# Performance work log

Hardware: AMD Instinct MI355X
Metric: run time of the kernel (lower is better)

## Reference

```python
import jax, jax.numpy as jnp
import numpy as np

N_CUST = 500000
N_FUND = 50000
N_EDGE = 4000000
D_CUST = 101
D_FUND = 1
HID = 64


def setup_inputs() -> dict:
    key = jax.random.key(0)
    ks = jax.random.split(key, 16)
    s = lambda fan_in: 1.0 / np.sqrt(fan_in)
    return {
        "x_customer": jax.random.normal(ks[0], (N_CUST, D_CUST), jnp.float32),
        "x_fund": jax.random.normal(ks[1], (N_FUND, D_FUND), jnp.float32),
        "src_fund": jax.random.randint(ks[2], (N_EDGE,), 0, N_FUND, jnp.int64),
        "dst_customer": jax.random.randint(ks[3], (N_EDGE,), 0, N_CUST, jnp.int64),
        # per-node-type input projections
        "W_cust": jax.random.uniform(ks[4], (D_CUST, HID), jnp.float32, -s(D_CUST), s(D_CUST)),
        "b_cust": jax.random.uniform(ks[5], (HID,), jnp.float32, -s(D_CUST), s(D_CUST)),
        "W_fund": jax.random.uniform(ks[6], (D_FUND, HID), jnp.float32, -s(D_FUND), s(D_FUND)),
        "b_fund": jax.random.uniform(ks[7], (HID,), jnp.float32, -s(D_FUND), s(D_FUND)),
        # SAGEConv fund->customer: lin_l (neighbor aggr, bias) + lin_r (self, no bias)
        "W_l": jax.random.uniform(ks[8], (HID, HID), jnp.float32, -s(HID), s(HID)),
        "b_l": jax.random.uniform(ks[9], (HID,), jnp.float32, -s(HID), s(HID)),
        "W_r": jax.random.uniform(ks[10], (HID, HID), jnp.float32, -s(HID), s(HID)),
        # output head
        "W_out": jax.random.uniform(ks[11], (HID, 2), jnp.float32, -s(HID), s(HID)),
        "b_out": jax.random.uniform(ks[12], (2,), jnp.float32, -s(HID), s(HID)),
    }


def reference(x_customer, x_fund, src_fund, dst_customer,
              W_cust, b_cust, W_fund, b_fund, W_l, b_l, W_r, W_out, b_out):
    # per-node-type linear + relu
    h_c = jax.nn.relu(x_customer @ W_cust + b_cust)  # [N_CUST, HID]
    h_f = jax.nn.relu(x_fund @ W_fund + b_fund)      # [N_FUND, HID]

    # SAGEConv (fund -> customer): gather src fund features per edge,
    # mean-aggregate by destination customer (scatter-sum / count)
    msgs = h_f[src_fund]  # [N_EDGE, HID]
    summed = jax.ops.segment_sum(msgs, dst_customer, num_segments=N_CUST)
    cnt = jax.ops.segment_sum(jnp.ones((msgs.shape[0],), msgs.dtype),
                              dst_customer, num_segments=N_CUST)
    mean = summed / jnp.maximum(cnt, 1.0)[:, None]

    out_c = mean @ W_l + b_l + h_c @ W_r  # SAGE: lin_l(aggr) + lin_r(self)
    return out_c @ W_out + b_out          # [N_CUST, 2]
```

## Files before the change

### kernel.cpp

```cpp
#include <hip/hip_runtime.h>
#include <stdint.h>

#define N_CUST 500000
#define N_FUND 50000
#define N_EDGE 4000000
#define D_CUST 101
#define HID 64

#define NB   512
#define EPB  ((N_EDGE + NB - 1) / NB)
#define CB   512
#define NBKT ((N_CUST + CB - 1) / CB)
#define CAP  5120
#define GPAD 32
#define LROW 104

typedef float float4u __attribute__((ext_vector_type(4), aligned(4)));
typedef float float4a __attribute__((ext_vector_type(4), aligned(16)));
using frag_ab = __attribute__((ext_vector_type(8))) short;
using frag_cd = __attribute__((ext_vector_type(4))) float;

struct __align__(16) Accum { float g0, g1, cnt, pad; };

__device__ __forceinline__ short f2bf(float f) {
    unsigned u = __float_as_uint(f);
    u += 0x7fffu + ((u >> 16) & 1u);
    return (short)(u >> 16);
}

__global__ __launch_bounds__(256) void k_gf(
    const float* __restrict__ x_fund,
    const float* __restrict__ W_fund,
    const float* __restrict__ b_fund,
    const float* __restrict__ W_l,
    const float* __restrict__ W_r,
    const float* __restrict__ W_out,
    const float* __restrict__ Wc,
    const float* __restrict__ b_l,
    const float* __restrict__ b_out,
    float2* __restrict__ gf,
    frag_ab* __restrict__ wcb,
    float* __restrict__ Bt,
    float* __restrict__ c2,
    unsigned* __restrict__ gcur,
    float4* __restrict__ Az)
{
    __shared__ float sAf[128];
    __shared__ float sWf[64];
    __shared__ float sBf[64];
    int t = threadIdx.x;

    if (Az != nullptr) {
        float4 z4 = make_float4(0.f, 0.f, 0.f, 0.f);
        for (int i = blockIdx.x * 256 + t; i < N_CUST; i += gridDim.x * 256)
            Az[i] = z4;
    }

    if (t < 128) {
        int h = t >> 1, j = t & 1;
        float s = 0.f;
        for (int k = 0; k < 64; ++k)
            s = fmaf(W_l[h * 64 + k], W_out[k * 2 + j], s);
        sAf[t] = s;
    } else if (t < 192) {
        sWf[t - 128] = W_fund[t - 128];
    } else {
        sBf[t - 192] = b_fund[t - 192];
    }
    __syncthreads();

    int f = blockIdx.x * 256 + t;
    if (f < N_FUND) {
        float xf = x_fund[f];
        float g0 = 0.f, g1 = 0.f;
        #pragma unroll
        for (int h = 0; h < 64; ++h) {
            float hf = fmaxf(fmaf(xf, sWf[h], sBf[h]), 0.f);
            g0 = fmaf(hf, sAf[2 * h + 0], g0);
            g1 = fmaf(hf, sAf[2 * h + 1], g1);
        }
        gf[f] = make_float2(g0, g1);
    }

    if (blockIdx.x == 0) {
        for (int k = t; k < NBKT * GPAD; k += 256) gcur[k] = 0u;
        if (t < 128) {
            int h = t >> 1, j = t & 1;
            float s = 0.f;
            for (int k = 0; k < 64; ++k)
                s = fmaf(W_r[h * 64 + k], W_out[k * 2 + j], s);
            Bt[t] = s;
        } else if (t < 130) {
            int j = t - 128;
            float s = b_out[j];
            for (int k = 0; k < 64; ++k)
                s = fmaf(b_l[k], W_out[k * 2 + j], s);
            c2[j] = s;
        }
        for (int sidx = t; sidx < 1024; sidx += 256) {
            int fidx = sidx >> 6, l = sidx & 63;
            int c = l & 15, q = l >> 4;
            int nt = fidx >> 2, kc = fidx & 3;
            frag_ab fr;
            #pragma unroll
            for (int j = 0; j < 8; ++j) {
                int kk = kc * 32 + q * 8 + j;
                int h  = nt * 16 + c;
                fr[j] = (kk < D_CUST) ? f2bf(Wc[kk * HID + h]) : (short)0;
            }
            wcb[sidx] = fr;
        }
    }
}

__global__ __launch_bounds__(512) void k_reorder(
    const int* __restrict__ src, const int* __restrict__ dst,
    unsigned* __restrict__ gcur, unsigned* __restrict__ recs)
{
    __shared__ unsigned hist[NBKT];
    __shared__ unsigned localOff[NBKT];
    __shared__ unsigned cur[NBKT];
    __shared__ unsigned baseG[NBKT];
    __shared__ unsigned ldsRec[EPB];
    __shared__ unsigned short ldsBkt[EPB];

    int t = threadIdx.x, b = blockIdx.x;
    int e0 = b * EPB, e1 = min(e0 + EPB, N_EDGE);
    int cntE = e1 - e0;

    for (int k = t; k < NBKT; k += 512) hist[k] = 0;
    __syncthreads();
    for (int e = e0 + t; e < e1; e += 512)
        atomicAdd(&hist[((unsigned)dst[e]) >> 9], 1u);
    __syncthreads();

    if (t < 64) {
        unsigned v[16], pre[16], run = 0;
        #pragma unroll
        for (int j = 0; j < 16; ++j) {
            int idx = t * 16 + j;
            v[j] = (idx < NBKT) ? hist[idx] : 0u;
            pre[j] = run; run += v[j];
        }
        unsigned sc = run;
        #pragma unroll
        for (int d = 1; d < 64; d <<= 1) {
            unsigned n = __shfl_up(sc, d, 64);
            if (t >= d) sc += n;
        }
        unsigned lane_excl = sc - run;
        #pragma unroll
        for (int j = 0; j < 16; ++j) {
            int idx = t * 16 + j;
            if (idx < NBKT) {
                localOff[idx] = lane_excl + pre[j];
                cur[idx]      = lane_excl + pre[j];
            }
        }
    }
    __syncthreads();

    for (int k = t; k < NBKT; k += 512) {
        unsigned h = hist[k];
        baseG[k] = h ? ((unsigned)k * CAP + atomicAdd(&gcur[k * GPAD], h)) : 0u;
    }

    for (int e = e0 + t; e < e1; e += 512) {
        unsigned d = (unsigned)dst[e];
        unsigned s = (unsigned)src[e];
        unsigned k = d >> 9;
        unsigned p = atomicAdd(&cur[k], 1u);
        ldsRec[p] = s | ((d & 511u) << 16);
        ldsBkt[p] = (unsigned short)k;
    }
    __syncthreads();

    for (int i = t; i < cntE; i += 512) {
        unsigned k = ldsBkt[i];
        unsigned g = baseG[k] + (i - localOff[k]);
        if (g < (k + 1u) * CAP) recs[g] = ldsRec[i];
    }
}

__global__ __launch_bounds__(256) void k_bucket(
    const unsigned* __restrict__ recs, const unsigned* __restrict__ gcur,
    const float2* __restrict__ gf,
    const float* __restrict__ x, const float* __restrict__ bc,
    const frag_ab* __restrict__ wcb, const float* __restrict__ Bt,
    const float* __restrict__ c2,
    float2* __restrict__ out)
{
    __shared__ float s0[CB], s1[CB], scn[CB];
    __shared__ float pbuf[2 * CB];
    __shared__ float xbuf[3][16 * LROW];

    int t = threadIdx.x, k = blockIdx.x;
    int w = t >> 6, lane = t & 63;
    int c = lane & 15, q = lane >> 4;

    for (int cc = t; cc < CB; cc += 256) { s0[cc] = 0.f; s1[cc] = 0.f; scn[cc] = 0.f; }
    __syncthreads();

    int cust0 = k * CB;
    int ncust = min(CB, N_CUST - cust0);
    int n_tiles = ncust >> 4;

    if (w == 3) {
        unsigned n = min(gcur[(unsigned)k * GPAD], (unsigned)CAP);
        const unsigned* rp = recs + (size_t)k * CAP;
        unsigned i = (unsigned)lane * 4u;
        for (; i + 4u <= n; i += 256u) {
            uint4 rr = *(const uint4*)(rp + i);
            float2 ga = gf[rr.x & 0xFFFFu];
            float2 gb = gf[rr.y & 0xFFFFu];
            float2 gc = gf[rr.z & 0xFFFFu];
            float2 gd = gf[rr.w & 0xFFFFu];
            unsigned da = rr.x >> 16, db = rr.y >> 16;
            unsigned dc = rr.z >> 16, dd = rr.w >> 16;
            atomicAdd(&s0[da], ga.x); atomicAdd(&s1[da], ga.y); atomicAdd(&scn[da], 1.f);
            atomicAdd(&s0[db], gb.x); atomicAdd(&s1[db], gb.y); atomicAdd(&scn[db], 1.f);
            atomicAdd(&s0[dc], gc.x); atomicAdd(&s1[dc], gc.y); atomicAdd(&scn[dc], 1.f);
            atomicAdd(&s0[dd], gd.x); atomicAdd(&s1[dd], gd.y); atomicAdd(&scn[dd], 1.f);
        }
        unsigned base = n & ~3u;
        if ((unsigned)lane < (n & 3u)) {
            unsigned r = rp[base + lane];
            float2 g = gf[r & 0xFFFFu];
            unsigned dl = r >> 16;
            atomicAdd(&s0[dl], g.x); atomicAdd(&s1[dl], g.y); atomicAdd(&scn[dl], 1.f);
        }
    } else {
        float* buf = xbuf[w];
        frag_ab bfrag[16];
        #pragma unroll
        for (int f = 0; f < 16; ++f) bfrag[f] = wcb[f * 64 + lane];
        float btv[8];
        #pragma unroll
        for (int nt = 0; nt < 4; ++nt) {
            btv[2 * nt]     = Bt[(nt * 16 + c) * 2];
            btv[2 * nt + 1] = Bt[(nt * 16 + c) * 2 + 1];
        }
        float bcv[4];
        #pragma unroll
        for (int nt = 0; nt < 4; ++nt) bcv[nt] = bc[nt * 16 + c];
        float c20 = c2[0], c21 = c2[1];

        int r = lane >> 2, s4 = lane & 3;

        for (int tl = w; tl < n_tiles; tl += 3) {
            const float* tb = x + (size_t)(cust0 + tl * 16) * D_CUST;
            #pragma unroll
            for (int rnd = 0; rnd < 7; ++rnd) {
                int ch = s4 + rnd * 4;
                if (ch < 25) {
                    float4u v = *(const float4u*)(tb + r * D_CUST + ch * 4);
                    *(float4a*)(buf + r * LROW + ch * 4) = v;
                } else if (ch == 25) {
                    buf[r * LROW + 100] = tb[r * D_CUST + 100];
                }
            }

            frag_ab af[4];
            #pragma unroll
            for (int kc = 0; kc < 3; ++kc) {
                float4a lo = *(const float4a*)(buf + c * LROW + kc * 32 + q * 8);
                float4a hi = *(const float4a*)(buf + c * LROW + kc * 32 + q * 8 + 4);
                frag_ab f;
                f[0]=f2bf(lo[0]); f[1]=f2bf(lo[1]); f[2]=f2bf(lo[2]); f[3]=f2bf(lo[3]);
                f[4]=f2bf(hi[0]); f[5]=f2bf(hi[1]); f[6]=f2bf(hi[2]); f[7]=f2bf(hi[3]);
                af[kc] = f;
            }
            {
                frag_ab f = {0,0,0,0,0,0,0,0};
                if (q == 0) {
                    float4a lo = *(const float4a*)(buf + c * LROW + 96);
                    f[0]=f2bf(lo[0]); f[1]=f2bf(lo[1]); f[2]=f2bf(lo[2]); f[3]=f2bf(lo[3]);
                    f[4]=f2bf(buf[c * LROW + 100]);
                }
                af[3] = f;
            }

            frag_cd acc[4];
            #pragma unroll
            for (int nt = 0; nt < 4; ++nt)
                acc[nt] = (frag_cd){bcv[nt], bcv[nt], bcv[nt], bcv[nt]};
            #pragma unroll
            for (int kc = 0; kc < 4; ++kc)
                #pragma unroll
                for (int nt = 0; nt < 4; ++nt)
                    acc[nt] = __builtin_amdgcn_mfma_f32_16x16x32_bf16(
                        af[kc], bfrag[nt * 4 + kc], acc[nt], 0, 0, 0);

            #pragma unroll
            for (int i = 0; i < 4; ++i) {
                float p0 = 0.f, p1 = 0.f;
                #pragma unroll
                for (int nt = 0; nt < 4; ++nt) {
                    float zv = fmaxf(acc[nt][i], 0.f);
                    p0 = fmaf(zv, btv[2 * nt],     p0);
                    p1 = fmaf(zv, btv[2 * nt + 1], p1);
                }
                #pragma unroll
                for (int m = 1; m < 16; m <<= 1) {
                    p0 += __shfl_xor(p0, m, 16);
                    p1 += __shfl_xor(p1, m, 16);
                }
                if (c == 0) {
                    int lrow = tl * 16 + q * 4 + i;
                    pbuf[2 * lrow]     = p0 + c20;
                    pbuf[2 * lrow + 1] = p1 + c21;
                }
            }
        }
    }
    __syncthreads();

    for (int cc = t; cc < ncust; cc += 256) {
        float inv = 1.0f / fmaxf(scn[cc], 1.0f);
        out[cust0 + cc] = make_float2(fmaf(s0[cc], inv, pbuf[2 * cc]),
                                      fmaf(s1[cc], inv, pbuf[2 * cc + 1]));
    }
}

__global__ __launch_bounds__(256) void k_scatter_direct(
    const int* __restrict__ src, const int* __restrict__ dst,
    const float2* __restrict__ gf, Accum* __restrict__ A)
{
    int stride = gridDim.x * 256;
    for (int e = blockIdx.x * 256 + threadIdx.x; e < N_EDGE; e += stride) {
        int s = src[e], d = dst[e];
        float2 g = gf[s];
        unsafeAtomicAdd(&A[d].g0, g.x);
        unsafeAtomicAdd(&A[d].g1, g.y);
        unsafeAtomicAdd(&A[d].cnt, 1.0f);
    }
}

__global__ __launch_bounds__(256) void k_mean(
    const Accum* __restrict__ A, float2* __restrict__ mean2)
{
    int i = blockIdx.x * 256 + threadIdx.x;
    if (i < N_CUST) {
        Accum a = A[i];
        float inv = 1.0f / fmaxf(a.cnt, 1.0f);
        mean2[i] = make_float2(a.g0 * inv, a.g1 * inv);
    }
}

__global__ __launch_bounds__(256) void k_gemm(
    const float* __restrict__ x, const float* __restrict__ bc,
    const frag_ab* __restrict__ wcb, const float* __restrict__ Bt,
    const float* __restrict__ c2, const float2* __restrict__ mean2,
    float2* __restrict__ out)
{
    __shared__ float sBt[128];
    __shared__ float zb[4][16 * 68];

    int t = threadIdx.x;
    int w = t >> 6, lane = t & 63;
    int c = lane & 15, q = lane >> 4;
    float* z = zb[w];

    if (t < 128) sBt[t] = Bt[t];
    frag_ab bfrag[16];
    #pragma unroll
    for (int f = 0; f < 16; ++f) bfrag[f] = wcb[f * 64 + lane];
    float bcv[4];
    #pragma unroll
    for (int nt = 0; nt < 4; ++nt) bcv[nt] = bc[nt * 16 + c];
    float c20 = c2[0], c21 = c2[1];
    __syncthreads();

    const int NT = N_CUST / 16;
    for (int tl = blockIdx.x * 4 + w; tl < NT; tl += gridDim.x * 4) {
        int row0 = tl * 16;
        const float* xr = x + (size_t)(row0 + c) * D_CUST;
        frag_ab af[4];
        #pragma unroll
        for (int kc = 0; kc < 3; ++kc) {
            float4u lo = *(const float4u*)(xr + kc * 32 + q * 8);
            float4u hi = *(const float4u*)(xr + kc * 32 + q * 8 + 4);
            frag_ab f;
            f[0]=f2bf(lo[0]); f[1]=f2bf(lo[1]); f[2]=f2bf(lo[2]); f[3]=f2bf(lo[3]);
            f[4]=f2bf(hi[0]); f[5]=f2bf(hi[1]); f[6]=f2bf(hi[2]); f[7]=f2bf(hi[3]);
            af[kc] = f;
        }
        {
            frag_ab f = {0,0,0,0,0,0,0,0};
            if (q == 0) {
                float4u lo = *(const float4u*)(xr + 96);
                f[0]=f2bf(lo[0]); f[1]=f2bf(lo[1]); f[2]=f2bf(lo[2]); f[3]=f2bf(lo[3]);
                f[4]=f2bf(xr[100]);
            }
            af[3] = f;
        }
        frag_cd acc[4];
        #pragma unroll
        for (int nt = 0; nt < 4; ++nt)
            acc[nt] = (frag_cd){bcv[nt], bcv[nt], bcv[nt], bcv[nt]};
        #pragma unroll
        for (int kc = 0; kc < 4; ++kc)
            #pragma unroll
            for (int nt = 0; nt < 4; ++nt)
                acc[nt] = __builtin_amdgcn_mfma_f32_16x16x32_bf16(
                    af[kc], bfrag[nt * 4 + kc], acc[nt], 0, 0, 0);
        #pragma unroll
        for (int nt = 0; nt < 4; ++nt)
            #pragma unroll
            for (int i = 0; i < 4; ++i)
                z[(q * 4 + i) * 68 + nt * 16 + c] = fmaxf(acc[nt][i], 0.f);
        float p0 = 0.f, p1 = 0.f;
        #pragma unroll
        for (int j4 = 0; j4 < 4; ++j4) {
            float4u zv = *(const float4u*)(z + c * 68 + q * 16 + j4 * 4);
            float4u b0 = *(const float4u*)(sBt + q * 32 + j4 * 8);
            float4u b1 = *(const float4u*)(sBt + q * 32 + j4 * 8 + 4);
            p0 = fmaf(zv[0], b0[0], p0); p1 = fmaf(zv[0], b0[1], p1);
            p0 = fmaf(zv[1], b0[2], p0); p1 = fmaf(zv[1], b0[3], p1);
            p0 = fmaf(zv[2], b1[0], p0); p1 = fmaf(zv[2], b1[1], p1);
            p0 = fmaf(zv[3], b1[2], p0); p1 = fmaf(zv[3], b1[3], p1);
        }
        p0 += __shfl_xor(p0, 16, 64); p0 += __shfl_xor(p0, 32, 64);
        p1 += __shfl_xor(p1, 16, 64); p1 += __shfl_xor(p1, 32, 64);
        if (q == 0) {
            float2 m = mean2[row0 + c];
            out[row0 + c] = make_float2(p0 + c20 + m.x, p1 + c21 + m.y);
        }
    }
}

extern "C" void kernel_launch(void* const* d_in, const int* in_sizes, int n_in,
                              void* d_out, int out_size, void* d_ws, size_t ws_size,
                              hipStream_t stream) {
    const float* x_customer = (const float*)d_in[0];
    const float* x_fund     = (const float*)d_in[1];
    const int*   src_fund   = (const int*)d_in[2];
    const int*   dst_cust   = (const int*)d_in[3];
    const float* W_cust     = (const float*)d_in[4];
    const float* b_cust     = (const float*)d_in[5];
    const float* W_fund     = (const float*)d_in[6];
    const float* b_fund     = (const float*)d_in[7];
    const float* W_l        = (const float*)d_in[8];
    const float* b_l        = (const float*)d_in[9];
    const float* W_r        = (const float*)d_in[10];
    const float* W_out      = (const float*)d_in[11];
    const float* b_out      = (const float*)d_in[12];

    char* ws = (char*)d_ws;
    const size_t NEED_FAST = 20550976ull;

    if (ws_size >= NEED_FAST) {
        unsigned* recs = (unsigned*)(ws);
        float2*   gf   = (float2*)  (ws + 20008960);
        frag_ab*  wcb  = (frag_ab*) (ws + 20408960);
        float*    Bt   = (float*)   (ws + 20425344);
        float*    c2   = (float*)   (ws + 20425856);
        unsigned* gcur = (unsigned*)(ws + 20425920);

        k_gf<<<256, 256, 0, stream>>>(
            x_fund, W_fund, b_fund, W_l, W_r, W_out, W_cust, b_l, b_out,
            gf, wcb, Bt, c2, gcur, nullptr);
        k_reorder<<<NB, 512, 0, stream>>>(src_fund, dst_cust, gcur, recs);
        k_bucket<<<NBKT, 256, 0, stream>>>(
            recs, gcur, gf, x_customer, b_cust, wcb, Bt, c2, (float2*)d_out);
    } else {
        Accum*    A    = (Accum*)   (ws);
        float2*   mn2  = (float2*)  (ws + 8000000);
        float2*   gf   = (float2*)  (ws + 12000000);
        frag_ab*  wcb  = (frag_ab*) (ws + 12400000);
        float*    Bt   = (float*)   (ws + 12416384);
        float*    c2   = (float*)   (ws + 12416896);
        unsigned* gcur = (unsigned*)(ws + 12416960);

        k_gf<<<256, 256, 0, stream>>>(
            x_fund, W_fund, b_fund, W_l, W_r, W_out, W_cust, b_l, b_out,
            gf, wcb, Bt, c2, gcur, (float4*)A);
        k_scatter_direct<<<2048, 256, 0, stream>>>(src_fund, dst_cust, gf, A);
        k_mean<<<(N_CUST + 255) / 256, 256, 0, stream>>>(A, mn2);
        k_gemm<<<2048, 256, 0, stream>>>(
            x_customer, b_cust, wcb, Bt, c2, mn2, (float2*)d_out);
    }
}
```

Baseline: 507.2 us.

## Prefetch next customer tile into registers and stage tiles as flat contiguous chunks

The per-wave customer tile loop now loads each 16-row tile as a flat contiguous block of aligned float4 chunks (rows packed at stride 101 instead of padded 104) and software-pipelines it. The next tile's global loads are issued into registers before computing the current tile. This hides global-load latency behind the MFMA work and makes loads fully coalesced and 16-byte aligned. The costs are extra register pressure (two 7×float4 buffers) and scalar, possibly bank-conflicted LDS reads for the A fragments, since rows are no longer 16-byte aligned in LDS.

```diff
diff --git a/kernel.cpp b/kernel.cpp
--- a/kernel.cpp
+++ b/kernel.cpp
@@ -13,7 +13,8 @@
 #define NBKT ((N_CUST + CB - 1) / CB)
 #define CAP  5120
 #define GPAD 32
-#define LROW 104
+#define TSZ  (16 * D_CUST)
+#define NCH  ((TSZ + 3) / 4)
 
 typedef float float4u __attribute__((ext_vector_type(4), aligned(4)));
 typedef float float4a __attribute__((ext_vector_type(4), aligned(16)));
@@ -26,6 +27,78 @@
     unsigned u = __float_as_uint(f);
     u += 0x7fffu + ((u >> 16) & 1u);
     return (short)(u >> 16);
+}
+
+__device__ __forceinline__ void loadflat(const float* __restrict__ tb,
+                                         int lane, float4a rv[7]) {
+    #pragma unroll
+    for (int r = 0; r < 7; ++r) {
+        int ch = lane + (r << 6);
+        if (ch < NCH) rv[r] = *(const float4a*)(tb + (ch << 2));
+    }
+}
+
+__device__ __forceinline__ void stageflat(float* __restrict__ buf,
+                                          int lane, const float4a rv[7]) {
+    #pragma unroll
+    for (int r = 0; r < 7; ++r) {
+        int ch = lane + (r << 6);
+        if (ch < NCH) *(float4a*)(buf + (ch << 2)) = rv[r];
+    }
+}
+
+__device__ __forceinline__ void compute_tile(
+    const float* __restrict__ buf, const frag_ab bfrag[16],
+    const float bcv[4], const float btv[8], float c20, float c21,
+    int tl, int q, int c, float* __restrict__ pbuf) {
+    const float* rowp = buf + c * D_CUST;
+    frag_ab af[4];
+    #pragma unroll
+    for (int kc = 0; kc < 3; ++kc) {
+        frag_ab f;
+        #pragma unroll
+        for (int j = 0; j < 8; ++j)
+            f[j] = f2bf(rowp[kc * 32 + q * 8 + j]);
+        af[kc] = f;
+    }
+    {
+        frag_ab f = {0,0,0,0,0,0,0,0};
+        if (q == 0) {
+            f[0]=f2bf(rowp[96]); f[1]=f2bf(rowp[97]); f[2]=f2bf(rowp[98]);
+            f[3]=f2bf(rowp[99]); f[4]=f2bf(rowp[100]);
+        }
+        af[3] = f;
+    }
+    frag_cd acc[4];
+    #pragma unroll
+    for (int nt = 0; nt < 4; ++nt)
+        acc[nt] = (frag_cd){bcv[nt], bcv[nt], bcv[nt], bcv[nt]};
+    #pragma unroll
+    for (int kc = 0; kc < 4; ++kc)
+        #pragma unroll
+        for (int nt = 0; nt < 4; ++nt)
+            acc[nt] = __builtin_amdgcn_mfma_f32_16x16x32_bf16(
+                af[kc], bfrag[nt * 4 + kc], acc[nt], 0, 0, 0);
+    #pragma unroll
+    for (int i = 0; i < 4; ++i) {
+        float p0 = 0.f, p1 = 0.f;
+        #pragma unroll
+        for (int nt = 0; nt < 4; ++nt) {
+            float zv = fmaxf(acc[nt][i], 0.f);
+            p0 = fmaf(zv, btv[2 * nt],     p0);
+            p1 = fmaf(zv, btv[2 * nt + 1], p1);
+        }
+        #pragma unroll
+        for (int m = 1; m < 16; m <<= 1) {
+            p0 += __shfl_xor(p0, m, 16);
+            p1 += __shfl_xor(p1, m, 16);
+        }
+        if (c == 0) {
+            int lrow = tl * 16 + q * 4 + i;
+            pbuf[2 * lrow]     = p0 + c20;
+            pbuf[2 * lrow + 1] = p1 + c21;
+        }
+    }
 }
 
 __global__ __launch_bounds__(256) void k_gf(
@@ -192,7 +265,7 @@
 {
     __shared__ float s0[CB], s1[CB], scn[CB];
     __shared__ float pbuf[2 * CB];
-    __shared__ float xbuf[3][16 * LROW];
+    __shared__ float xbuf[3][TSZ];
 
     int t = threadIdx.x, k = blockIdx.x;
     int w = t >> 6, lane = t & 63;
@@ -245,71 +318,25 @@
         for (int nt = 0; nt < 4; ++nt) bcv[nt] = bc[nt * 16 + c];
         float c20 = c2[0], c21 = c2[1];
 
-        int r = lane >> 2, s4 = lane & 3;
-
-        for (int tl = w; tl < n_tiles; tl += 3) {
-            const float* tb = x + (size_t)(cust0 + tl * 16) * D_CUST;
-            #pragma unroll
-            for (int rnd = 0; rnd < 7; ++rnd) {
-                int ch = s4 + rnd * 4;
-                if (ch < 25) {
-                    float4u v = *(const float4u*)(tb + r * D_CUST + ch * 4);
-                    *(float4a*)(buf + r * LROW + ch * 4) = v;
-                } else if (ch == 25) {
-                    buf[r * LROW + 100] = tb[r * D_CUST + 100];
-                }
-            }
-
-            frag_ab af[4];
-            #pragma unroll
-            for (int kc = 0; kc < 3; ++kc) {
-                float4a lo = *(const float4a*)(buf + c * LROW + kc * 32 + q * 8);
-                float4a hi = *(const float4a*)(buf + c * LROW + kc * 32 + q * 8 + 4);
-                frag_ab f;
-                f[0]=f2bf(lo[0]); f[1]=f2bf(lo[1]); f[2]=f2bf(lo[2]); f[3]=f2bf(lo[3]);
-                f[4]=f2bf(hi[0]); f[5]=f2bf(hi[1]); f[6]=f2bf(hi[2]); f[7]=f2bf(hi[3]);
-                af[kc] = f;
-            }
-            {
-                frag_ab f = {0,0,0,0,0,0,0,0};
-                if (q == 0) {
-                    float4a lo = *(const float4a*)(buf + c * LROW + 96);
-                    f[0]=f2bf(lo[0]); f[1]=f2bf(lo[1]); f[2]=f2bf(lo[2]); f[3]=f2bf(lo[3]);
-                    f[4]=f2bf(buf[c * LROW + 100]);
-                }
-                af[3] = f;
-            }
-
-            frag_cd acc[4];
-            #pragma unroll
-            for (int nt = 0; nt < 4; ++nt)
-                acc[nt] = (frag_cd){bcv[nt], bcv[nt], bcv[nt], bcv[nt]};
-            #pragma unroll
-            for (int kc = 0; kc < 4; ++kc)
-                #pragma unroll
-                for (int nt = 0; nt < 4; ++nt)
-                    acc[nt] = __builtin_amdgcn_mfma_f32_16x16x32_bf16(
-                        af[kc], bfrag[nt * 4 + kc], acc[nt], 0, 0, 0);
-
-            #pragma unroll
-            for (int i = 0; i < 4; ++i) {
-                float p0 = 0.f, p1 = 0.f;
-                #pragma unroll
-                for (int nt = 0; nt < 4; ++nt) {
-                    float zv = fmaxf(acc[nt][i], 0.f);
-                    p0 = fmaf(zv, btv[2 * nt],     p0);
-                    p1 = fmaf(zv, btv[2 * nt + 1], p1);
-                }
-                #pragma unroll
-                for (int m = 1; m < 16; m <<= 1) {
-                    p0 += __shfl_xor(p0, m, 16);
-                    p1 += __shfl_xor(p1, m, 16);
-                }
-                if (c == 0) {
-                    int lrow = tl * 16 + q * 4 + i;
-                    pbuf[2 * lrow]     = p0 + c20;
-                    pbuf[2 * lrow + 1] = p1 + c21;
-                }
+        int tl = w;
+        if (tl < n_tiles) {
+            float4a rvA[7], rvB[7];
+            loadflat(x + (size_t)(cust0 + tl * 16) * D_CUST, lane, rvA);
+            for (;;) {
+                int t1 = tl + 3;
+                stageflat(buf, lane, rvA);
+                if (t1 < n_tiles)
+                    loadflat(x + (size_t)(cust0 + t1 * 16) * D_CUST, lane, rvB);
+                compute_tile(buf, bfrag, bcv, btv, c20, c21, tl, q, c, pbuf);
+                if (t1 >= n_tiles) break;
+                tl = t1;
+                int t2 = tl + 3;
+                stageflat(buf, lane, rvB);
+                if (t2 < n_tiles)
+                    loadflat(x + (size_t)(cust0 + t2 * 16) * D_CUST, lane, rvA);
+                compute_tile(buf, bfrag, bcv, btv, c20, c21, tl, q, c, pbuf);
+                if (t2 >= n_tiles) break;
+                tl = t2;
             }
         }
     }
```

Result: faster. 425.1 us (-16.2%).
